# Performance work log

Hardware: AMD Instinct MI355X
Metric: run time of the kernel (lower is better)

The kernel has to match this reference:

```python
import jax, jax.numpy as jnp
import numpy as np

EPS = float(np.finfo(np.float64).eps)  # np.finfo(float).eps as in torch combine


def setup_inputs() -> dict:
    key = jax.random.key(0)
    ks = jax.random.split(key, 4)
    B, E, D_in, D_h, D_out = 4096, 8, 768, 2048, 768
    return {
        "x": jax.random.normal(ks[0], (B, D_in), dtype=jnp.float32),
        "w_gate": jax.random.normal(ks[1], (D_in, E), dtype=jnp.float32) * 0.02,
        "W1": jax.random.normal(ks[2], (E, D_in, D_h), dtype=jnp.float32) * (1.0 / np.sqrt(D_in)),
        "b1": jnp.zeros((E, D_h), dtype=jnp.float32),
        "W2": jax.random.normal(ks[3], (E, D_h, D_out), dtype=jnp.float32) * (1.0 / np.sqrt(D_h)),
        "b2": jnp.zeros((E, D_out), dtype=jnp.float32),
        "k": 2,
    }


def _cv_squared(v):
    # torch .var() is unbiased (ddof=1)
    return jnp.var(v, ddof=1) / (jnp.mean(v) ** 2 + 1e-10)


def _top_k_gates(logits, k):
    B, E = logits.shape
    top_vals, top_idx = jax.lax.top_k(logits, k)        # [B, k]
    top_gates = jax.nn.softmax(top_vals, axis=1)        # softmax over the k kept logits
    gates = jnp.zeros((B, E), logits.dtype).at[jnp.arange(B)[:, None], top_idx].set(top_gates)
    return gates


def reference(x, w_gate, W1, b1, W2, b2, k):
    # --- gating (eval path: noiseless clean logits, softmax gating) ---
    logits = x @ w_gate                                  # [B, E]
    gates = _top_k_gates(logits, k)                      # [B, E], sparse (k nonzeros/row)
    # --- per-expert MLP: Linear -> gelu -> Linear -> log_softmax ---
    # Dense grouped compute over experts; gate==0 terms contribute nothing in combine.
    h = jax.nn.gelu(jnp.einsum('bi,eih->beh', x, W1) + b1[None])      # [B, E, Dh]
    lo = jax.nn.log_softmax(jnp.einsum('beh,eho->beo', h, W2) + b2[None], axis=-1)  # [B, E, Do]
    # --- combine: exp, weight by gates, scatter-add, eps-clamp, log ---
    combined = jnp.einsum('be,beo->bo', gates, jnp.exp(lo))           # [B, Do]
    y = jnp.log(jnp.where(combined == 0, EPS, combined))
    # --- load-balancing aux loss (eval: load = count of nonzero gates) ---
    importance = gates.sum(0)
    load = (gates > 0).sum(0).astype(jnp.float32)
    loss = 0.01 * (_cv_squared(importance) + _cv_squared(load))
    return y, loss
```

## Files before the change

kernel.cpp:

```cpp
#include <hip/hip_runtime.h>
#include <hip/hip_bf16.h>
#include <math.h>

typedef __hip_bfloat16 bf16;
typedef short v8s __attribute__((ext_vector_type(8)));
typedef float v4f __attribute__((ext_vector_type(4)));

#define B_TOK 4096
#define E_EXP 8
#define D_IN  768
#define D_H   2048
#define D_OUT 768
#define MAXT  72

__device__ __forceinline__ void gl_lds16(const bf16* g, bf16* l) {
  __builtin_amdgcn_global_load_lds(
      (const __attribute__((address_space(1))) unsigned int*)g,
      (__attribute__((address_space(3))) unsigned int*)l, 16, 0, 0);
}

__global__ void gate_cvt_kernel(const float* __restrict__ x, const float* __restrict__ wg,
                                bf16* __restrict__ xb,
                                float* __restrict__ gates, int* __restrict__ tidx) {
  int gt = blockIdx.x * 256 + threadIdx.x;
  int tok = gt >> 6, l = gt & 63;
  const float* xr = x + (size_t)tok * D_IN;
  bf16* xbr = xb + (size_t)tok * D_IN;
  float acc[8] = {0.f,0.f,0.f,0.f,0.f,0.f,0.f,0.f};
  #pragma unroll
  for (int i = 0; i < 3; ++i) {
    int k0 = i * 256 + l * 4;
    float4 v = *(const float4*)(xr + k0);
    union { bf16 h[4]; uint2 u; } pk;
    pk.h[0] = __float2bfloat16(v.x); pk.h[1] = __float2bfloat16(v.y);
    pk.h[2] = __float2bfloat16(v.z); pk.h[3] = __float2bfloat16(v.w);
    *(uint2*)(xbr + k0) = pk.u;
    float xv[4] = {v.x, v.y, v.z, v.w};
    #pragma unroll
    for (int j = 0; j < 4; ++j) {
      const float* wr = wg + (size_t)(k0 + j) * 8;
      float4 w0 = *(const float4*)wr;
      float4 w1 = *(const float4*)(wr + 4);
      acc[0] += xv[j] * w0.x; acc[1] += xv[j] * w0.y;
      acc[2] += xv[j] * w0.z; acc[3] += xv[j] * w0.w;
      acc[4] += xv[j] * w1.x; acc[5] += xv[j] * w1.y;
      acc[6] += xv[j] * w1.z; acc[7] += xv[j] * w1.w;
    }
  }
  #pragma unroll
  for (int d = 1; d < 64; d <<= 1)
    #pragma unroll
    for (int e = 0; e < 8; ++e) acc[e] += __shfl_xor(acc[e], d);
  if (l == 0) {
    int i1 = 0; float v1 = acc[0];
    #pragma unroll
    for (int e = 1; e < 8; ++e) if (acc[e] > v1) { v1 = acc[e]; i1 = e; }
    int i2 = -1; float v2 = -1e30f;
    #pragma unroll
    for (int e = 0; e < 8; ++e) if (e != i1 && acc[e] > v2) { v2 = acc[e]; i2 = e; }
    float ex = __expf(v2 - v1);
    float g1 = 1.f / (1.f + ex), g2 = ex / (1.f + ex);
    gates[2 * tok] = g1; gates[2 * tok + 1] = g2;
    tidx[2 * tok] = i1;  tidx[2 * tok + 1] = i2;
  }
}

__global__ void finalize_kernel(const int* __restrict__ tidx, const float* __restrict__ gates,
                                int* __restrict__ cnt_off, int* __restrict__ row_ids,
                                int* __restrict__ pos, int* __restrict__ tmap,
                                float* __restrict__ loss_out) {
  __shared__ int   hcnt[256][9];
  __shared__ float himp[256][9];
  __shared__ int   tot[8], off[8];
  __shared__ float itot[8];
  int t = threadIdx.x;
  #pragma unroll
  for (int e = 0; e < 8; ++e) { hcnt[t][e] = 0; himp[t][e] = 0.f; }
  __syncthreads();
  for (int i = 0; i < 32; ++i) {
    int idx = t * 32 + i;
    int e = tidx[idx];
    hcnt[t][e] += 1;
    himp[t][e] += gates[idx];
  }
  __syncthreads();
  if (t < 8) {
    int run = 0; float s = 0.f;
    for (int j = 0; j < 256; ++j) {
      int c = hcnt[j][t];
      hcnt[j][t] = run;
      run += c;
      s += himp[j][t];
    }
    tot[t] = run; itot[t] = s;
  }
  __syncthreads();
  if (t == 0) {
    int o = 0;
    float mi = 0.f, ml = 0.f;
    for (int e = 0; e < 8; ++e) {
      off[e] = o; o += tot[e];
      cnt_off[e] = tot[e]; cnt_off[8 + e] = off[e];
      mi += itot[e]; ml += (float)tot[e];
    }
    mi *= 0.125f; ml *= 0.125f;
    float vi = 0.f, vl = 0.f;
    for (int e = 0; e < 8; ++e) {
      float d = itot[e] - mi;        vi += d * d;
      float d2 = (float)tot[e] - ml; vl += d2 * d2;
    }
    vi /= 7.f; vl /= 7.f;
    *loss_out = 0.01f * (vi / (mi * mi + 1e-10f) + vl / (ml * ml + 1e-10f));
    int nt = 0;
    for (int e = 0; e < 8; ++e)
      for (int tt = 0; tt < (tot[e] + 127) >> 7; ++tt) {
        tmap[nt] = e; tmap[MAXT + nt] = tt; ++nt;
      }
    for (; nt < MAXT; ++nt) tmap[nt] = -1;
  }
  __syncthreads();
  for (int i = 0; i < 32; ++i) {
    int idx = t * 32 + i;
    int e = tidx[idx];
    int slot = off[e] + hcnt[t][e];
    hcnt[t][e] += 1;
    row_ids[slot] = idx >> 1;
    pos[idx] = slot;
  }
}

__global__ void transpose_cvt(const float* __restrict__ W, bf16* __restrict__ Wt,
                              int K, int N) {
  __shared__ bf16 tile[64][72];
  int e = blockIdx.z;
  int k0 = blockIdx.y * 64, n0 = blockIdx.x * 64;
  const float* Wp = W + (size_t)e * K * N;
  bf16* Wtp = Wt + (size_t)e * N * K;
  int t = threadIdx.x;
  int cr = t >> 4;
  int cc = (t & 15) * 4;
  #pragma unroll
  for (int p = 0; p < 4; ++p) {
    int kr = cr + p * 16;
    float4 v = *(const float4*)(Wp + (size_t)(k0 + kr) * N + n0 + cc);
    tile[cc + 0][kr] = __float2bfloat16(v.x);
    tile[cc + 1][kr] = __float2bfloat16(v.y);
    tile[cc + 2][kr] = __float2bfloat16(v.z);
    tile[cc + 3][kr] = __float2bfloat16(v.w);
  }
  __syncthreads();
  #pragma unroll
  for (int p = 0; p < 2; ++p) {
    int o = p * 256 + t;
    int n = o >> 3, k8 = (o & 7) * 8;
    v8s val = *(const v8s*)&tile[n][k8];
    *(v8s*)(Wtp + (size_t)(n0 + n) * K + k0 + k8) = val;
  }
}

template<int KDIM, bool GATHER, bool GELU>
__global__ __launch_bounds__(256)
void gemm_mlp(const bf16* __restrict__ Ab, const bf16* __restrict__ Wt,
              const float* __restrict__ bias, bf16* __restrict__ Outb,
              const int* __restrict__ row_ids, const int* __restrict__ cnt_off,
              const int* __restrict__ tmap, const int N) {
  constexpr int BK = 64, BM = 128, BN = 128;
  constexpr int NK = KDIM / BK;
  static_assert(NK % 4 == 0, "NK multiple of 4");
  __shared__ __align__(16) bf16 lds[4][2][BM * BK];
  const int ti = blockIdx.y;
  const int e = tmap[ti];
  if (e < 0) return;
  const int rowb = tmap[MAXT + ti];
  const int cnt = cnt_off[e];
  const int off = cnt_off[8 + e];
  const int colb = blockIdx.x;
  const int t = (int)threadIdx.x, w = t >> 6, l = t & 63;
  const int cs = (l & 7) ^ (l >> 3);
  const bf16* gA[4];
  const bf16* gB[4];
  #pragma unroll
  for (int it = 0; it < 4; ++it) {
    int rt = (it * 4 + w) * 8 + (l >> 3);
    int r = rowb * BM + rt;
    int rc = r < cnt ? r : cnt - 1;
    long arow = GATHER ? (long)row_ids[off + rc] : (long)(off + rc);
    gA[it] = Ab + arow * (long)KDIM + cs * 8;
  }
  #pragma unroll
  for (int it = 0; it < 4; ++it) {
    int rt = (it * 4 + w) * 8 + (l >> 3);
    gB[it] = Wt + ((size_t)e * N + (size_t)colb * BN + rt) * KDIM + cs * 8;
  }
  v4f acc[4][4] = {};
  const int wm = w >> 1, wn = w & 1;

#define STAGE(b, k0) do {                                                   \
    _Pragma("unroll")                                                       \
    for (int it = 0; it < 4; ++it)                                          \
      gl_lds16(gA[it] + (k0), &lds[b][0][(it * 4 + w) * 512]);              \
    _Pragma("unroll")                                                       \
    for (int it = 0; it < 4; ++it)                                          \
      gl_lds16(gB[it] + (k0), &lds[b][1][(it * 4 + w) * 512]);              \
  } while (0)

#define COMPUTE(b) do {                                                     \
    _Pragma("unroll")                                                       \
    for (int kk = 0; kk < 2; ++kk) {                                        \
      v8s af[4], bfr[4];                                                    \
      _Pragma("unroll")                                                     \
      for (int fm = 0; fm < 4; ++fm) {                                      \
        int row = wm * 64 + fm * 16 + (l & 15);                             \
        int cg = kk * 4 + (l >> 4);                                         \
        af[fm] = *(const v8s*)(&lds[b][0][0] + row * BK + ((cg ^ (row & 7)) << 3)); \
      }                                                                     \
      _Pragma("unroll")                                                     \
      for (int fn = 0; fn < 4; ++fn) {                                      \
        int row = wn * 64 + fn * 16 + (l & 15);                             \
        int cg = kk * 4 + (l >> 4);                                         \
        bfr[fn] = *(const v8s*)(&lds[b][1][0] + row * BK + ((cg ^ (row & 7)) << 3)); \
      }                                                                     \
      _Pragma("unroll")                                                     \
      for (int fm = 0; fm < 4; ++fm)                                        \
        _Pragma("unroll")                                                   \
        for (int fn = 0; fn < 4; ++fn)                                      \
          acc[fm][fn] = __builtin_amdgcn_mfma_f32_16x16x32_bf16(af[fm], bfr[fn], acc[fm][fn], 0, 0, 0); \
    }                                                                       \
  } while (0)

#define PIPE_STEP(j, kn, VMS) do {                                          \
    if ((kn) < NK) STAGE((j + 3) & 3, (kn) * BK);                           \
    asm volatile("s_waitcnt " VMS ::: "memory");                            \
    __builtin_amdgcn_sched_barrier(0);                                      \
    __builtin_amdgcn_s_barrier();                                           \
    __builtin_amdgcn_sched_barrier(0);                                      \
    COMPUTE(j);                                                             \
    __builtin_amdgcn_s_barrier();                                           \
    __builtin_amdgcn_sched_barrier(0);                                      \
  } while (0)

  STAGE(0, 0); STAGE(1, BK); STAGE(2, 2 * BK);
  #pragma unroll 1
  for (int i4 = 0; i4 < NK - 4; i4 += 4) {
    PIPE_STEP(0, i4 + 3, "vmcnt(24)");
    PIPE_STEP(1, i4 + 4, "vmcnt(24)");
    PIPE_STEP(2, i4 + 5, "vmcnt(24)");
    PIPE_STEP(3, i4 + 6, "vmcnt(24)");
  }
  PIPE_STEP(0, NK - 1, "vmcnt(24)");
  PIPE_STEP(1, NK,     "vmcnt(16)");
  PIPE_STEP(2, NK + 1, "vmcnt(8)");
  PIPE_STEP(3, NK + 2, "vmcnt(0)");
#undef STAGE
#undef COMPUTE
#undef PIPE_STEP

  float* eps = (float*)(&lds[0][0][0]) + w * (16 * 68);
  const float* bp = bias + (size_t)e * N + (size_t)colb * BN + wn * 64 + (l & 7) * 8;
  float bv[8];
  #pragma unroll
  for (int jj = 0; jj < 8; ++jj) bv[jj] = bp[jj];
  #pragma unroll
  for (int fm = 0; fm < 4; ++fm) {
    #pragma unroll
    for (int fn = 0; fn < 4; ++fn)
      #pragma unroll
      for (int q = 0; q < 4; ++q)
        eps[((l >> 4) * 4 + q) * 68 + fn * 16 + (l & 15)] = acc[fm][fn][q];
    #pragma unroll
    for (int half = 0; half < 2; ++half) {
      int row = (l >> 3) + 8 * half;
      int r = rowb * BM + wm * 64 + fm * 16 + row;
      if (r < cnt) {
        const float* rp = eps + row * 68 + (l & 7) * 8;
        union { bf16 h[8]; uint4 u; } pk;
        #pragma unroll
        for (int jj = 0; jj < 8; ++jj) {
          float v = rp[jj] + bv[jj];
          if (GELU) {
            float u = 0.7978845608028654f * (v + 0.044715f * v * v * v);
            float th = 1.f - 2.f / (__expf(2.f * u) + 1.f);
            v = 0.5f * v * (1.f + th);
          }
          pk.h[jj] = __float2bfloat16(v);
        }
        *(uint4*)(Outb + (size_t)(off + r) * N + (size_t)colb * BN + wn * 64 + (l & 7) * 8) = pk.u;
      }
    }
  }
}

__global__ void combine_kernel(const bf16* __restrict__ z, const float* __restrict__ gates,
                               const int* __restrict__ pos, float* __restrict__ y) {
  int gt = blockIdx.x * 256 + threadIdx.x;
  int tok = gt >> 6, l = gt & 63;
  if (tok >= B_TOK) return;
  const bf16* z1 = z + (size_t)pos[2 * tok] * D_OUT;
  const bf16* z2 = z + (size_t)pos[2 * tok + 1] * D_OUT;
  float g1 = gates[2 * tok], g2 = gates[2 * tok + 1];
  float a[12], b[12];
  float m1 = -1e30f, m2 = -1e30f;
  #pragma unroll
  for (int i = 0; i < 12; ++i) {
    a[i] = __bfloat162float(z1[l + 64 * i]);
    b[i] = __bfloat162float(z2[l + 64 * i]);
    m1 = fmaxf(m1, a[i]); m2 = fmaxf(m2, b[i]);
  }
  #pragma unroll
  for (int d = 1; d < 64; d <<= 1) {
    m1 = fmaxf(m1, __shfl_xor(m1, d));
    m2 = fmaxf(m2, __shfl_xor(m2, d));
  }
  float s1 = 0.f, s2 = 0.f;
  #pragma unroll
  for (int i = 0; i < 12; ++i) { s1 += __expf(a[i] - m1); s2 += __expf(b[i] - m2); }
  #pragma unroll
  for (int d = 1; d < 64; d <<= 1) { s1 += __shfl_xor(s1, d); s2 += __shfl_xor(s2, d); }
  float c1 = g1 / s1, c2 = g2 / s2;
  #pragma unroll
  for (int i = 0; i < 12; ++i) {
    float cmb = c1 * __expf(a[i] - m1) + c2 * __expf(b[i] - m2);
    y[(size_t)tok * D_OUT + l + 64 * i] = logf(cmb == 0.f ? 2.2204460492503131e-16f : cmb);
  }
}

extern "C" void kernel_launch(void* const* d_in, const int* in_sizes, int n_in,
                              void* d_out, int out_size, void* d_ws, size_t ws_size,
                              hipStream_t stream) {
  const float* x  = (const float*)d_in[0];
  const float* wg = (const float*)d_in[1];
  const float* W1 = (const float*)d_in[2];
  const float* b1 = (const float*)d_in[3];
  const float* W2 = (const float*)d_in[4];
  const float* b2 = (const float*)d_in[5];
  float* out = (float*)d_out;

  char* ws = (char*)d_ws;
  int*   cnt_off = (int*)(ws + 0);
  float* gates   = (float*)(ws + 256);
  int*   tidx    = (int*)(ws + 256 + 32768);
  int*   pos     = (int*)(ws + 256 + 65536);
  int*   row_ids = (int*)(ws + 256 + 98304);
  int*   tmap    = (int*)(ws + 256 + 131072);
  const size_t base = 262144;
  bf16* x_bf = (bf16*)(ws + base);
  bf16* W1t  = (bf16*)(ws + base + 6291456);
  bf16* W2t  = (bf16*)(ws + base + 31457280);
  bf16* h_bf = (bf16*)(ws + base + 56623104);
  bf16* z_bf = (bf16*)(ws + base);

  transpose_cvt<<<dim3(D_H / 64,  D_IN / 64, E_EXP), 256, 0, stream>>>(W1, W1t, D_IN, D_H);
  transpose_cvt<<<dim3(D_OUT / 64, D_H / 64, E_EXP), 256, 0, stream>>>(W2, W2t, D_H, D_OUT);
  gate_cvt_kernel<<<dim3(1024), 256, 0, stream>>>(x, wg, x_bf, gates, tidx);
  finalize_kernel<<<dim3(1), 256, 0, stream>>>(tidx, gates, cnt_off, row_ids, pos, tmap,
                                               out + (size_t)B_TOK * D_OUT);
  gemm_mlp<D_IN, true,  true ><<<dim3(D_H / 128,  MAXT), 256, 0, stream>>>(
      x_bf, W1t, b1, h_bf, row_ids, cnt_off, tmap, D_H);
  gemm_mlp<D_H,  false, false><<<dim3(D_OUT / 128, MAXT), 256, 0, stream>>>(
      h_bf, W2t, b2, z_bf, row_ids, cnt_off, tmap, D_OUT);
  combine_kernel<<<dim3(1024), 256, 0, stream>>>(z_bf, gates, pos, out);
}
```

Before: 177.3 us.

## Enlarge GEMM tiles to 256-wide with 512 threads and double-buffered pipeline

Grows the expert GEMM tiles to BN=256, with BM=256 for the first GEMM and BM=128 for the second, and runs them on 512-thread blocks with 8 waves. The LDS pipeline drops from four stages to two, and s_setprio is raised around the MFMA sections. A second tile map is added so each GEMM gets its own row-tile count. The larger tiles aim to cut global and LDS traffic per FLOP and to reuse more data per block. In exchange there are fewer blocks, which hurts load balance across the CUs, and the shallower prefetch depth may expose memory latency.

Result: faster. 170.7 us (-3.8%).

```diff
diff --git a/kernel.cpp b/kernel.cpp
--- a/kernel.cpp
+++ b/kernel.cpp
@@ -11,7 +11,8 @@
 #define D_IN  768
 #define D_H   2048
 #define D_OUT 768
-#define MAXT  72
+#define MAXTA 40
+#define MAXTB 72
 
 __device__ __forceinline__ void gl_lds16(const bf16* g, bf16* l) {
   __builtin_amdgcn_global_load_lds(
@@ -67,8 +68,8 @@
 
 __global__ void finalize_kernel(const int* __restrict__ tidx, const float* __restrict__ gates,
                                 int* __restrict__ cnt_off, int* __restrict__ row_ids,
-                                int* __restrict__ pos, int* __restrict__ tmap,
-                                float* __restrict__ loss_out) {
+                                int* __restrict__ pos, int* __restrict__ tmapA,
+                                int* __restrict__ tmapB, float* __restrict__ loss_out) {
   __shared__ int   hcnt[256][9];
   __shared__ float himp[256][9];
   __shared__ int   tot[8], off[8];
@@ -113,10 +114,16 @@
     *loss_out = 0.01f * (vi / (mi * mi + 1e-10f) + vl / (ml * ml + 1e-10f));
     int nt = 0;
     for (int e = 0; e < 8; ++e)
+      for (int tt = 0; tt < (tot[e] + 255) >> 8; ++tt) {
+        tmapA[nt] = e; tmapA[MAXTA + nt] = tt; ++nt;
+      }
+    for (; nt < MAXTA; ++nt) tmapA[nt] = -1;
+    nt = 0;
+    for (int e = 0; e < 8; ++e)
       for (int tt = 0; tt < (tot[e] + 127) >> 7; ++tt) {
-        tmap[nt] = e; tmap[MAXT + nt] = tt; ++nt;
+        tmapB[nt] = e; tmapB[MAXTB + nt] = tt; ++nt;
       }
-    for (; nt < MAXT; ++nt) tmap[nt] = -1;
+    for (; nt < MAXTB; ++nt) tmapB[nt] = -1;
   }
   __syncthreads();
   for (int i = 0; i < 32; ++i) {
@@ -158,30 +165,32 @@
   }
 }
 
-template<int KDIM, bool GATHER, bool GELU>
-__global__ __launch_bounds__(256)
+template<int KDIM, int BM, bool GATHER, bool GELU>
+__global__ __launch_bounds__(512, 2)
 void gemm_mlp(const bf16* __restrict__ Ab, const bf16* __restrict__ Wt,
               const float* __restrict__ bias, bf16* __restrict__ Outb,
               const int* __restrict__ row_ids, const int* __restrict__ cnt_off,
-              const int* __restrict__ tmap, const int N) {
-  constexpr int BK = 64, BM = 128, BN = 128;
+              const int* __restrict__ tmap, const int maxt, const int N) {
+  constexpr int BK = 64, BN = 256;
   constexpr int NK = KDIM / BK;
-  static_assert(NK % 4 == 0, "NK multiple of 4");
-  __shared__ __align__(16) bf16 lds[4][2][BM * BK];
+  constexpr int ITA = BM / 64;
+  constexpr int FM  = BM / 32;
+  static_assert(NK % 2 == 0 && NK >= 4, "NK even, >=4");
+  __shared__ __align__(16) bf16 lds[2][(BM + BN) * BK];
   const int ti = blockIdx.y;
   const int e = tmap[ti];
   if (e < 0) return;
-  const int rowb = tmap[MAXT + ti];
+  const int rowb = tmap[maxt + ti];
   const int cnt = cnt_off[e];
   const int off = cnt_off[8 + e];
   const int colb = blockIdx.x;
   const int t = (int)threadIdx.x, w = t >> 6, l = t & 63;
   const int cs = (l & 7) ^ (l >> 3);
-  const bf16* gA[4];
+  const bf16* gA[ITA];
   const bf16* gB[4];
   #pragma unroll
-  for (int it = 0; it < 4; ++it) {
-    int rt = (it * 4 + w) * 8 + (l >> 3);
+  for (int it = 0; it < ITA; ++it) {
+    int rt = (it * 8 + w) * 8 + (l >> 3);
     int r = rowb * BM + rt;
     int rc = r < cnt ? r : cnt - 1;
     long arow = GATHER ? (long)row_ids[off + rc] : (long)(off + rc);
@@ -189,79 +198,82 @@
   }
   #pragma unroll
   for (int it = 0; it < 4; ++it) {
-    int rt = (it * 4 + w) * 8 + (l >> 3);
+    int rt = (it * 8 + w) * 8 + (l >> 3);
     gB[it] = Wt + ((size_t)e * N + (size_t)colb * BN + rt) * KDIM + cs * 8;
   }
-  v4f acc[4][4] = {};
-  const int wm = w >> 1, wn = w & 1;
+  v4f acc[FM][4] = {};
+  const int wm = w >> 2, wn = w & 3;
 
 #define STAGE(b, k0) do {                                                   \
     _Pragma("unroll")                                                       \
-    for (int it = 0; it < 4; ++it)                                          \
-      gl_lds16(gA[it] + (k0), &lds[b][0][(it * 4 + w) * 512]);              \
+    for (int it = 0; it < ITA; ++it)                                        \
+      gl_lds16(gA[it] + (k0), &lds[b][(it * 8 + w) * 512]);                 \
     _Pragma("unroll")                                                       \
     for (int it = 0; it < 4; ++it)                                          \
-      gl_lds16(gB[it] + (k0), &lds[b][1][(it * 4 + w) * 512]);              \
+      gl_lds16(gB[it] + (k0), &lds[b][BM * BK + (it * 8 + w) * 512]);       \
   } while (0)
 
 #define COMPUTE(b) do {                                                     \
+    __builtin_amdgcn_s_setprio(1);                                          \
     _Pragma("unroll")                                                       \
     for (int kk = 0; kk < 2; ++kk) {                                        \
-      v8s af[4], bfr[4];                                                    \
+      v8s af[FM], bfr[4];                                                   \
       _Pragma("unroll")                                                     \
-      for (int fm = 0; fm < 4; ++fm) {                                      \
-        int row = wm * 64 + fm * 16 + (l & 15);                             \
+      for (int fm = 0; fm < FM; ++fm) {                                     \
+        int row = wm * (BM / 2) + fm * 16 + (l & 15);                       \
         int cg = kk * 4 + (l >> 4);                                         \
-        af[fm] = *(const v8s*)(&lds[b][0][0] + row * BK + ((cg ^ (row & 7)) << 3)); \
+        af[fm] = *(const v8s*)(&lds[b][0] + row * BK + ((cg ^ (row & 7)) << 3)); \
       }                                                                     \
       _Pragma("unroll")                                                     \
       for (int fn = 0; fn < 4; ++fn) {                                      \
         int row = wn * 64 + fn * 16 + (l & 15);                             \
         int cg = kk * 4 + (l >> 4);                                         \
-        bfr[fn] = *(const v8s*)(&lds[b][1][0] + row * BK + ((cg ^ (row & 7)) << 3)); \
+        bfr[fn] = *(const v8s*)(&lds[b][BM * BK] + row * BK + ((cg ^ (row & 7)) << 3)); \
       }                                                                     \
       _Pragma("unroll")                                                     \
-      for (int fm = 0; fm < 4; ++fm)                                        \
+      for (int fm = 0; fm < FM; ++fm)                                       \
         _Pragma("unroll")                                                   \
         for (int fn = 0; fn < 4; ++fn)                                      \
           acc[fm][fn] = __builtin_amdgcn_mfma_f32_16x16x32_bf16(af[fm], bfr[fn], acc[fm][fn], 0, 0, 0); \
     }                                                                       \
+    __builtin_amdgcn_s_setprio(0);                                          \
   } while (0)
 
-#define PIPE_STEP(j, kn, VMS) do {                                          \
-    if ((kn) < NK) STAGE((j + 3) & 3, (kn) * BK);                           \
-    asm volatile("s_waitcnt " VMS ::: "memory");                            \
-    __builtin_amdgcn_sched_barrier(0);                                      \
-    __builtin_amdgcn_s_barrier();                                           \
-    __builtin_amdgcn_sched_barrier(0);                                      \
-    COMPUTE(j);                                                             \
-    __builtin_amdgcn_s_barrier();                                           \
-    __builtin_amdgcn_sched_barrier(0);                                      \
-  } while (0)
-
-  STAGE(0, 0); STAGE(1, BK); STAGE(2, 2 * BK);
+#define SB   __builtin_amdgcn_sched_barrier(0)
+#define BARR __builtin_amdgcn_s_barrier()
+#define WAITLPT do { if (ITA == 4) asm volatile("s_waitcnt vmcnt(8)" ::: "memory"); \
+                     else          asm volatile("s_waitcnt vmcnt(6)" ::: "memory"); } while (0)
+#define WAITZ  asm volatile("s_waitcnt vmcnt(0)" ::: "memory")
+
+  STAGE(0, 0);
   #pragma unroll 1
-  for (int i4 = 0; i4 < NK - 4; i4 += 4) {
-    PIPE_STEP(0, i4 + 3, "vmcnt(24)");
-    PIPE_STEP(1, i4 + 4, "vmcnt(24)");
-    PIPE_STEP(2, i4 + 5, "vmcnt(24)");
-    PIPE_STEP(3, i4 + 6, "vmcnt(24)");
-  }
-  PIPE_STEP(0, NK - 1, "vmcnt(24)");
-  PIPE_STEP(1, NK,     "vmcnt(16)");
-  PIPE_STEP(2, NK + 1, "vmcnt(8)");
-  PIPE_STEP(3, NK + 2, "vmcnt(0)");
+  for (int ks = 0; ks < NK - 2; ks += 2) {
+    STAGE(1, (ks + 1) * BK);
+    WAITLPT; SB; BARR; SB;
+    COMPUTE(0);
+    BARR; SB;
+    STAGE(0, (ks + 2) * BK);
+    WAITLPT; SB; BARR; SB;
+    COMPUTE(1);
+    BARR; SB;
+  }
+  STAGE(1, (NK - 1) * BK);
+  WAITLPT; SB; BARR; SB;
+  COMPUTE(0);
+  WAITZ; SB; BARR; SB;
+  COMPUTE(1);
 #undef STAGE
 #undef COMPUTE
-#undef PIPE_STEP
-
-  float* eps = (float*)(&lds[0][0][0]) + w * (16 * 68);
+#undef WAITLPT
+#undef WAITZ
+
+  float* eps = (float*)(&lds[0][0]) + w * (16 * 68);
   const float* bp = bias + (size_t)e * N + (size_t)colb * BN + wn * 64 + (l & 7) * 8;
   float bv[8];
   #pragma unroll
   for (int jj = 0; jj < 8; ++jj) bv[jj] = bp[jj];
   #pragma unroll
-  for (int fm = 0; fm < 4; ++fm) {
+  for (int fm = 0; fm < FM; ++fm) {
     #pragma unroll
     for (int fn = 0; fn < 4; ++fn)
       #pragma unroll
@@ -270,7 +282,7 @@
     #pragma unroll
     for (int half = 0; half < 2; ++half) {
       int row = (l >> 3) + 8 * half;
-      int r = rowb * BM + wm * 64 + fm * 16 + row;
+      int r = rowb * BM + wm * (BM / 2) + fm * 16 + row;
       if (r < cnt) {
         const float* rp = eps + row * 68 + (l & 7) * 8;
         union { bf16 h[8]; uint4 u; } pk;
@@ -288,6 +300,8 @@
       }
     }
   }
+#undef SB
+#undef BARR
 }
 
 __global__ void combine_kernel(const bf16* __restrict__ z, const float* __restrict__ gates,
@@ -341,7 +355,8 @@
   int*   tidx    = (int*)(ws + 256 + 32768);
   int*   pos     = (int*)(ws + 256 + 65536);
   int*   row_ids = (int*)(ws + 256 + 98304);
-  int*   tmap    = (int*)(ws + 256 + 131072);
+  int*   tmapA   = (int*)(ws + 256 + 131072);
+  int*   tmapB   = tmapA + 2 * MAXTA;
   const size_t base = 262144;
   bf16* x_bf = (bf16*)(ws + base);
   bf16* W1t  = (bf16*)(ws + base + 6291456);
@@ -352,11 +367,11 @@
   transpose_cvt<<<dim3(D_H / 64,  D_IN / 64, E_EXP), 256, 0, stream>>>(W1, W1t, D_IN, D_H);
   transpose_cvt<<<dim3(D_OUT / 64, D_H / 64, E_EXP), 256, 0, stream>>>(W2, W2t, D_H, D_OUT);
   gate_cvt_kernel<<<dim3(1024), 256, 0, stream>>>(x, wg, x_bf, gates, tidx);
-  finalize_kernel<<<dim3(1), 256, 0, stream>>>(tidx, gates, cnt_off, row_ids, pos, tmap,
-                                               out + (size_t)B_TOK * D_OUT);
-  gemm_mlp<D_IN, true,  true ><<<dim3(D_H / 128,  MAXT), 256, 0, stream>>>(
-      x_bf, W1t, b1, h_bf, row_ids, cnt_off, tmap, D_H);
-  gemm_mlp<D_H,  false, false><<<dim3(D_OUT / 128, MAXT), 256, 0, stream>>>(
-      h_bf, W2t, b2, z_bf, row_ids, cnt_off, tmap, D_OUT);
+  finalize_kernel<<<dim3(1), 256, 0, stream>>>(tidx, gates, cnt_off, row_ids, pos,
+                                               tmapA, tmapB, out + (size_t)B_TOK * D_OUT);
+  gemm_mlp<D_IN, 256, true,  true ><<<dim3(D_H / 256,  MAXTA), 512, 0, stream>>>(
+      x_bf, W1t, b1, h_bf, row_ids, cnt_off, tmapA, MAXTA, D_H);
+  gemm_mlp<D_H,  128, false, false><<<dim3(D_OUT / 256, MAXTB), 512, 0, stream>>>(
+      h_bf, W2t, b2, z_bf, row_ids, cnt_off, tmapB, MAXTB, D_OUT);
   combine_kernel<<<dim3(1024), 256, 0, stream>>>(z_bf, gates, pos, out);
 }
```

## Cut GEMM LDS pipeline to double buffering so two blocks fit per CU

Applied to the files above, without the earlier changes.

Replaces the 4-stage global-to-LDS pipeline (128 KB of LDS per block) with a 2-stage ping-pong buffer (64 KB) and sets launch bounds to request two blocks per CU. More resident blocks are meant to hide memory latency through occupancy instead of deep in-block prefetching. MFMA compute phases are also wrapped in s_setprio so waves that are computing get issue priority. The trade-off is less prefetch distance inside each block and a possibly tighter register budget.

After: 162.5 us. 1.09x faster.

```diff
diff --git a/kernel.cpp b/kernel.cpp
--- a/kernel.cpp
+++ b/kernel.cpp
@@ -159,15 +159,15 @@
 }
 
 template<int KDIM, bool GATHER, bool GELU>
-__global__ __launch_bounds__(256)
+__global__ __launch_bounds__(256, 2)
 void gemm_mlp(const bf16* __restrict__ Ab, const bf16* __restrict__ Wt,
               const float* __restrict__ bias, bf16* __restrict__ Outb,
               const int* __restrict__ row_ids, const int* __restrict__ cnt_off,
               const int* __restrict__ tmap, const int N) {
   constexpr int BK = 64, BM = 128, BN = 128;
   constexpr int NK = KDIM / BK;
-  static_assert(NK % 4 == 0, "NK multiple of 4");
-  __shared__ __align__(16) bf16 lds[4][2][BM * BK];
+  static_assert(NK % 2 == 0 && NK >= 4, "NK even, >=4");
+  __shared__ __align__(16) bf16 lds[2][(BM + BN) * BK];
   const int ti = blockIdx.y;
   const int e = tmap[ti];
   if (e < 0) return;
@@ -198,13 +198,14 @@
 #define STAGE(b, k0) do {                                                   \
     _Pragma("unroll")                                                       \
     for (int it = 0; it < 4; ++it)                                          \
-      gl_lds16(gA[it] + (k0), &lds[b][0][(it * 4 + w) * 512]);              \
+      gl_lds16(gA[it] + (k0), &lds[b][(it * 4 + w) * 512]);                 \
     _Pragma("unroll")                                                       \
     for (int it = 0; it < 4; ++it)                                          \
-      gl_lds16(gB[it] + (k0), &lds[b][1][(it * 4 + w) * 512]);              \
+      gl_lds16(gB[it] + (k0), &lds[b][BM * BK + (it * 4 + w) * 512]);       \
   } while (0)
 
 #define COMPUTE(b) do {                                                     \
+    __builtin_amdgcn_s_setprio(1);                                          \
     _Pragma("unroll")                                                       \
     for (int kk = 0; kk < 2; ++kk) {                                        \
       v8s af[4], bfr[4];                                                    \
@@ -212,13 +213,13 @@
       for (int fm = 0; fm < 4; ++fm) {                                      \
         int row = wm * 64 + fm * 16 + (l & 15);                             \
         int cg = kk * 4 + (l >> 4);                                         \
-        af[fm] = *(const v8s*)(&lds[b][0][0] + row * BK + ((cg ^ (row & 7)) << 3)); \
+        af[fm] = *(const v8s*)(&lds[b][0] + row * BK + ((cg ^ (row & 7)) << 3)); \
       }                                                                     \
       _Pragma("unroll")                                                     \
       for (int fn = 0; fn < 4; ++fn) {                                      \
         int row = wn * 64 + fn * 16 + (l & 15);                             \
         int cg = kk * 4 + (l >> 4);                                         \
-        bfr[fn] = *(const v8s*)(&lds[b][1][0] + row * BK + ((cg ^ (row & 7)) << 3)); \
+        bfr[fn] = *(const v8s*)(&lds[b][BM * BK] + row * BK + ((cg ^ (row & 7)) << 3)); \
       }                                                                     \
       _Pragma("unroll")                                                     \
       for (int fm = 0; fm < 4; ++fm)                                        \
@@ -226,36 +227,37 @@
         for (int fn = 0; fn < 4; ++fn)                                      \
           acc[fm][fn] = __builtin_amdgcn_mfma_f32_16x16x32_bf16(af[fm], bfr[fn], acc[fm][fn], 0, 0, 0); \
     }                                                                       \
+    __builtin_amdgcn_s_setprio(0);                                          \
   } while (0)
 
-#define PIPE_STEP(j, kn, VMS) do {                                          \
-    if ((kn) < NK) STAGE((j + 3) & 3, (kn) * BK);                           \
-    asm volatile("s_waitcnt " VMS ::: "memory");                            \
-    __builtin_amdgcn_sched_barrier(0);                                      \
-    __builtin_amdgcn_s_barrier();                                           \
-    __builtin_amdgcn_sched_barrier(0);                                      \
-    COMPUTE(j);                                                             \
-    __builtin_amdgcn_s_barrier();                                           \
-    __builtin_amdgcn_sched_barrier(0);                                      \
-  } while (0)
-
-  STAGE(0, 0); STAGE(1, BK); STAGE(2, 2 * BK);
+#define SB    __builtin_amdgcn_sched_barrier(0)
+#define BARR  __builtin_amdgcn_s_barrier()
+#define WAIT8 asm volatile("s_waitcnt vmcnt(8)" ::: "memory")
+#define WAITZ asm volatile("s_waitcnt vmcnt(0)" ::: "memory")
+
+  STAGE(0, 0);
   #pragma unroll 1
-  for (int i4 = 0; i4 < NK - 4; i4 += 4) {
-    PIPE_STEP(0, i4 + 3, "vmcnt(24)");
-    PIPE_STEP(1, i4 + 4, "vmcnt(24)");
-    PIPE_STEP(2, i4 + 5, "vmcnt(24)");
-    PIPE_STEP(3, i4 + 6, "vmcnt(24)");
-  }
-  PIPE_STEP(0, NK - 1, "vmcnt(24)");
-  PIPE_STEP(1, NK,     "vmcnt(16)");
-  PIPE_STEP(2, NK + 1, "vmcnt(8)");
-  PIPE_STEP(3, NK + 2, "vmcnt(0)");
+  for (int ks = 0; ks < NK - 2; ks += 2) {
+    STAGE(1, (ks + 1) * BK);
+    WAIT8; SB; BARR; SB;
+    COMPUTE(0);
+    BARR; SB;
+    STAGE(0, (ks + 2) * BK);
+    WAIT8; SB; BARR; SB;
+    COMPUTE(1);
+    BARR; SB;
+  }
+  STAGE(1, (NK - 1) * BK);
+  WAIT8; SB; BARR; SB;
+  COMPUTE(0);
+  WAITZ; SB; BARR; SB;
+  COMPUTE(1);
 #undef STAGE
 #undef COMPUTE
-#undef PIPE_STEP
-
-  float* eps = (float*)(&lds[0][0][0]) + w * (16 * 68);
+#undef WAIT8
+#undef WAITZ
+
+  float* eps = (float*)(&lds[0][0]) + w * (16 * 68);
   const float* bp = bias + (size_t)e * N + (size_t)colb * BN + wn * 64 + (l & 7) * 8;
   float bv[8];
   #pragma unroll
@@ -288,6 +290,8 @@
       }
     }
   }
+#undef SB
+#undef BARR
 }
 
 __global__ void combine_kernel(const bf16* __restrict__ z, const float* __restrict__ gates,
```
